# Optimization experiments

Measured on AMD Instinct MI355X. Metric: run time of the kernel, lower is better.

Reference implementation:

```python
import jax, jax.numpy as jnp
import numpy as np

BETA = 0.25

def setup_inputs() -> dict:
    key = jax.random.key(0)
    kz, ke = jax.random.split(key)
    z = jax.random.normal(kz, (8, 256, 8, 32, 32), dtype=jnp.float32)
    num_codes, code_dim = 1024, 256
    # matches nn.init.uniform_(weight, -1/num_codes, 1/num_codes) in scale
    embed = jax.random.uniform(ke, (num_codes, code_dim), dtype=jnp.float32,
                               minval=-1.0 / num_codes, maxval=1.0 / num_codes)
    return {"z": z, "embed": embed}


def reference(z, embed):
    # z: (B, C, D, H, W); embed: (num_codes, code_dim) with C == code_dim
    B, C, D, H, W = z.shape
    num_codes = embed.shape[0]
    z_flat = jnp.transpose(z, (0, 2, 3, 4, 1)).reshape(-1, C)  # (N, C)

    # squared euclidean distances to all codes: ||z||^2 + ||e||^2 - 2 z.e
    dist = ((z_flat * z_flat).sum(axis=1, keepdims=True)
            + (embed * embed).sum(axis=1)
            - 2.0 * z_flat @ embed.T)  # (N, num_codes)
    indices = jnp.argmin(dist, axis=1)  # (N,) int
    z_q_flat = embed[indices]  # (N, C) gather

    # commitment loss (codebook is EMA-updated, so only beta * commitment)
    commitment = jnp.mean((z_flat - jax.lax.stop_gradient(z_q_flat)) ** 2)
    loss = BETA * commitment

    # straight-through estimator
    z_q_flat = z_flat + jax.lax.stop_gradient(z_q_flat - z_flat)
    z_q = jnp.transpose(z_q_flat.reshape(B, D, H, W, C), (0, 4, 1, 2, 3))

    # perplexity (scatter-add histogram instead of materializing one-hot)
    counts = jnp.zeros((num_codes,), dtype=z.dtype).at[indices].add(1.0)
    avg_probs = counts / indices.shape[0]
    perplexity = jnp.exp(-jnp.sum(avg_probs * jnp.log(avg_probs + 1e-10)))

    return z_q, indices.reshape(B, D, H, W), loss, perplexity
```

## Files before the change

### kernel.cpp

```cpp
#include <hip/hip_runtime.h>
#include <math.h>

#define Cdim   256
#define Ssp    8192
#define Npts   65536
#define NCODES 1024
#define BETA   0.25f
#define MT     128
#define NKC    48
#define ESCALE 8192.0f
#define WS_NEED (65536 + (size_t)786432 * 2)

typedef _Float16 f16;
typedef f16   half8  __attribute__((ext_vector_type(8)));
typedef float f32x16 __attribute__((ext_vector_type(16)));

#define MFMA16(A, B, C) __builtin_amdgcn_mfma_f32_32x32x16_f16(A, B, C, 0, 0, 0)

__global__ __launch_bounds__(256) void enorm_kernel(const float* __restrict__ embed,
                                                    float* __restrict__ enorm) {
    int j = blockIdx.x * 256 + threadIdx.x;
    if (j >= NCODES) return;
    const float4* row = reinterpret_cast<const float4*>(embed + (size_t)j * Cdim);
    float s = 0.f;
#pragma unroll 8
    for (int c4 = 0; c4 < Cdim / 4; ++c4) {
        float4 v = row[c4];
        s += v.x * v.x + v.y * v.y + v.z * v.z + v.w * v.w;
    }
    enorm[j] = s;
}

__global__ __launch_bounds__(256) void prep_kernel(const float* __restrict__ embed,
                                                   f16* __restrict__ Bws) {
    int tid = blockIdx.x * 256 + threadIdx.x;
    int o4 = tid * 4;
    int kc = o4 >> 14;
    int r  = o4 & 16383;
    int j  = r >> 4;
    int k0 = r & 15;
#pragma unroll
    for (int i = 0; i < 4; ++i) {
        int k = kc * 16 + k0 + i;
        int c = k & 255;
        float ev = embed[j * 256 + c] * ESCALE;
        f16 eh = (f16)ev;
        f16 v  = (k >= 256 && k < 512) ? (f16)(ev - (float)eh) : eh;
        Bws[o4 + i] = v;
    }
}

#define GG(k) (((k) < 16) ? (2 * (k) + kb) : ((k) < 32) ? (2 * ((k) - 16) + kb) \
                                                        : (32 + 2 * ((k) - 32) + kb))

__global__ __launch_bounds__(512, 2) void vq_gemm(const float* __restrict__ z,
                                                  const f16* __restrict__ Bws,
                                                  const float* __restrict__ enorm,
                                                  float* __restrict__ out_idx,
                                                  float* __restrict__ loss_acc,
                                                  float* __restrict__ counts) {
    __shared__ __attribute__((aligned(16))) f16 As[MT * 512];
    __shared__ float en_s[NCODES];
    __shared__ float znp[4 * MT];
    __shared__ float zn_s[MT];
    __shared__ float redv[8 * MT];
    __shared__ int   redi[8 * MT];

    const int t  = threadIdx.x;
    const int l  = t & 63;
    const int w  = t >> 6;
    const int wm = w >> 2;
    const int wn = w & 3;
    const int ln = l & 31;
    const int kb = l >> 5;
    const int n0 = blockIdx.x * MT;
    const int b  = n0 >> 13;
    const int s0 = n0 & 8191;

    {
        const int p = t & 127;
        const int q = t >> 7;
        const float* zb = z + (size_t)b * ((size_t)Cdim * Ssp) + s0;
        float zsq = 0.f;
#pragma unroll
        for (int gi = 0; gi < 8; ++gi) {
            const int c0 = q * 64 + gi * 8;
            half8 hh, ll;
#pragma unroll
            for (int u = 0; u < 8; ++u) {
                float zv = zb[(size_t)(c0 + u) * Ssp + p];
                zsq += zv * zv;
                f16 zh = (f16)zv;
                hh[u] = zh;
                ll[u] = (f16)(zv - (float)zh);
            }
            const int g0 = c0 >> 3;
            *(half8*)&As[p * 512 + 8 * (g0 ^ (p & 7))]        = hh;
            *(half8*)&As[p * 512 + 8 * ((32 + g0) ^ (p & 7))] = ll;
        }
        znp[q * MT + p] = zsq;
    }
    for (int i = t; i < NCODES; i += 512) en_s[i] = enorm[i];
    __syncthreads();
    if (t < MT)
        zn_s[t] = ((znp[t] + znp[MT + t]) + znp[2 * MT + t]) + znp[3 * MT + t];
    __syncthreads();

#pragma unroll 1
    for (int jh = 0; jh < 2; ++jh) {
        f32x16 acc[2][4] = {};
        const f16* bbase = Bws + (size_t)(jh * 512 + wn * 128 + ln) * 16 + kb * 8;

        half8 b0 = *(const half8*)(bbase);
        half8 b1 = *(const half8*)(bbase + 512);
        half8 b2 = *(const half8*)(bbase + 1024);
        half8 b3 = *(const half8*)(bbase + 1536);

        const int rowA = wm * 64 + ln;
#pragma unroll 2
        for (int kc = 0; kc < NKC; ++kc) {
            const int gg  = GG(kc);
            const int gsw = 8 * (gg ^ (ln & 7));
            half8 a0 = *(const half8*)&As[rowA * 512 + gsw];
            half8 a1 = *(const half8*)&As[(rowA + 32) * 512 + gsw];

            half8 n0r = b0, n1 = b1, n2 = b2, n3 = b3;
            if (kc + 1 < NKC) {
                const f16* src = bbase + (size_t)(kc + 1) * 16384;
                n0r = *(const half8*)(src);
                n1  = *(const half8*)(src + 512);
                n2  = *(const half8*)(src + 1024);
                n3  = *(const half8*)(src + 1536);
            }
            acc[0][0] = MFMA16(a0, b0, acc[0][0]);
            acc[1][0] = MFMA16(a1, b0, acc[1][0]);
            acc[0][1] = MFMA16(a0, b1, acc[0][1]);
            acc[1][1] = MFMA16(a1, b1, acc[1][1]);
            acc[0][2] = MFMA16(a0, b2, acc[0][2]);
            acc[1][2] = MFMA16(a1, b2, acc[1][2]);
            acc[0][3] = MFMA16(a0, b3, acc[0][3]);
            acc[1][3] = MFMA16(a1, b3, acc[1][3]);
            b0 = n0r; b1 = n1; b2 = n2; b3 = n3;
        }

        const int h = l >> 5;
#pragma unroll
        for (int mm = 0; mm < 2; ++mm) {
#pragma unroll
            for (int rg = 0; rg < 16; ++rg) {
                const int row = wm * 64 + mm * 32 + (rg & 3) + 8 * (rg >> 2) + 4 * h;
                const float znv = zn_s[row];
                float bv = 3.0e38f; int bi = 0;
#pragma unroll
                for (int nn = 0; nn < 4; ++nn) {
                    const int col = jh * 512 + wn * 128 + nn * 32 + ln;
                    float k1 = znv + en_s[col];
                    float sc = k1 - acc[mm][nn][rg] * (2.0f / ESCALE);
                    if (sc < bv) { bv = sc; bi = col; }
                }
#pragma unroll
                for (int off = 1; off < 32; off <<= 1) {
                    float ov = __shfl_xor(bv, off, 64);
                    int   oi = __shfl_xor(bi, off, 64);
                    if (ov < bv || (ov == bv && oi < bi)) { bv = ov; bi = oi; }
                }
                if (ln == 0) {
                    redv[(jh * 4 + wn) * MT + row] = bv;
                    redi[(jh * 4 + wn) * MT + row] = bi;
                }
            }
        }
    }
    __syncthreads();

    if (t < MT) {
        float bv = redv[t]; int bi = redi[t];
#pragma unroll
        for (int s = 1; s < 8; ++s) {
            float ov = redv[s * MT + t]; int oi = redi[s * MT + t];
            if (ov < bv || (ov == bv && oi < bi)) { bv = ov; bi = oi; }
        }
        out_idx[n0 + t] = (float)bi;
        atomicAdd(&counts[bi], 1.0f);
        float lsum = bv;
#pragma unroll
        for (int off = 32; off > 0; off >>= 1) lsum += __shfl_down(lsum, off, 64);
        if ((t & 63) == 0) atomicAdd(loss_acc, lsum);
    }
}

__global__ __launch_bounds__(256) void vq_epi(const float* __restrict__ embed,
                                              const float* __restrict__ out_idx,
                                              float* __restrict__ out_zq) {
    const int n = blockIdx.x * 256 + threadIdx.x;
    const int b = n >> 13, s = n & 8191;
    const int idx = (int)out_idx[n];
    const float4* er = reinterpret_cast<const float4*>(embed + (size_t)idx * Cdim);
    float* oq = out_zq + (size_t)b * ((size_t)Cdim * Ssp) + s;
#pragma unroll 4
    for (int c4 = 0; c4 < Cdim / 4; ++c4) {
        float4 e = er[c4];
        const int c = c4 * 4;
        __builtin_nontemporal_store(e.x, oq + (size_t)(c + 0) * Ssp);
        __builtin_nontemporal_store(e.y, oq + (size_t)(c + 1) * Ssp);
        __builtin_nontemporal_store(e.z, oq + (size_t)(c + 2) * Ssp);
        __builtin_nontemporal_store(e.w, oq + (size_t)(c + 3) * Ssp);
    }
}

#define PTS 64
#define CT  128
#define KC  32
__global__ __launch_bounds__(256, 2) void vq_main_fb(const float* __restrict__ z,
                                                     const float* __restrict__ embed,
                                                     const float* __restrict__ enorm,
                                                     float* __restrict__ out_zq,
                                                     float* __restrict__ out_idx,
                                                     float* __restrict__ loss_acc,
                                                     float* __restrict__ counts) {
    __shared__ __attribute__((aligned(16))) float smem[Cdim * PTS + KC * CT];
    float* zt = smem;
    float* et = smem + Cdim * PTS;
    const int t  = threadIdx.x;
    const int n0 = blockIdx.x * PTS;
    const int b  = n0 >> 13;
    const int s0 = n0 & 8191;
    const float* zb = z + (size_t)b * Cdim * Ssp + s0;
    {
        const int p4 = (t & 15) * 4, crow = t >> 4;
#pragma unroll
        for (int it = 0; it < 16; ++it) {
            int c = it * 16 + crow;
            float4 v = *reinterpret_cast<const float4*>(zb + (size_t)c * Ssp + p4);
            *reinterpret_cast<float4*>(&zt[c * PTS + p4]) = v;
        }
    }
    __syncthreads();
    {
        const int p = t & 63, qq = t >> 6;
        float sacc = 0.f;
#pragma unroll 8
        for (int c = qq * 64; c < qq * 64 + 64; ++c) { float v = zt[c * PTS + p]; sacc += v * v; }
        et[qq * 64 + p] = sacc;
    }
    __syncthreads();
    const int pg = t & 15, jg = t >> 4;
    const int p0 = pg * 4;
    float zn[4];
#pragma unroll
    for (int i = 0; i < 4; ++i) {
        int p = p0 + i;
        zn[i] = ((et[p] + et[64 + p]) + et[128 + p]) + et[192 + p];
    }
    float bestv[4] = {3.0e38f, 3.0e38f, 3.0e38f, 3.0e38f};
    int   besti[4] = {0, 0, 0, 0};
    const int dj = t >> 3, q = t & 7;
    const int sw_st = (q & 3) << 3;
    for (int jt = 0; jt < NCODES / CT; ++jt) {
        const int J0 = jt * CT;
        float acc[4][8];
#pragma unroll
        for (int i = 0; i < 4; ++i)
#pragma unroll
            for (int m = 0; m < 8; ++m) acc[i][m] = 0.f;
        for (int ks = 0; ks < Cdim / KC; ++ks) {
            const int cc0 = ks * KC;
            __syncthreads();
#pragma unroll
            for (int i = 0; i < 4; ++i) {
                const int jrel = dj + 32 * i;
                const float4 v = *reinterpret_cast<const float4*>(
                    embed + (size_t)(J0 + jrel) * Cdim + cc0 + q * 4);
                const int c0 = q * 4;
                const int jsw = jrel ^ sw_st;
                et[(c0 + 0) * CT + jsw] = v.x;
                et[(c0 + 1) * CT + jsw] = v.y;
                et[(c0 + 2) * CT + jsw] = v.z;
                et[(c0 + 3) * CT + jsw] = v.w;
            }
            __syncthreads();
#pragma unroll 4
            for (int c = 0; c < KC; ++c) {
                const float4 zp = *reinterpret_cast<const float4*>(&zt[(cc0 + c) * PTS + p0]);
                const int jb = (jg * 8) ^ (((c >> 2) & 3) << 3);
                const float4 ea = *reinterpret_cast<const float4*>(&et[c * CT + jb]);
                const float4 eb = *reinterpret_cast<const float4*>(&et[c * CT + jb + 4]);
                const float zc[4] = {zp.x, zp.y, zp.z, zp.w};
                const float ec[8] = {ea.x, ea.y, ea.z, ea.w, eb.x, eb.y, eb.z, eb.w};
#pragma unroll
                for (int i = 0; i < 4; ++i)
#pragma unroll
                    for (int m = 0; m < 8; ++m) acc[i][m] += zc[i] * ec[m];
            }
        }
#pragma unroll
        for (int m = 0; m < 8; ++m) {
            const int cid = J0 + jg * 8 + m;
            const float en = enorm[cid];
#pragma unroll
            for (int i = 0; i < 4; ++i) {
                float k1 = zn[i] + en;
                float sc = k1 - 2.0f * acc[i][m];
                if (sc < bestv[i]) { bestv[i] = sc; besti[i] = cid; }
            }
        }
    }
    __syncthreads();
    float* rv = et; int* ri = (int*)(et + 1024); int* idxf = (int*)(et + 2048);
#pragma unroll
    for (int i = 0; i < 4; ++i) { int p = p0 + i; rv[p * 16 + jg] = bestv[i]; ri[p * 16 + jg] = besti[i]; }
    __syncthreads();
    if (t < PTS) {
        int p = t;
        float bv = rv[p * 16]; int bi = ri[p * 16];
        for (int g = 1; g < 16; ++g) {
            float v = rv[p * 16 + g]; int ii = ri[p * 16 + g];
            if (v < bv || (v == bv && ii < bi)) { bv = v; bi = ii; }
        }
        idxf[p] = bi;
        out_idx[n0 + p] = (float)bi;
        atomicAdd(&counts[bi], 1.0f);
    }
    __syncthreads();
    float lsum = 0.f;
    {
        const int p = t & 63, cbase = t >> 6;
        const int myidx = idxf[p];
        const float4* erow4 = reinterpret_cast<const float4*>(embed + (size_t)myidx * Cdim);
        float* ob = out_zq + (size_t)b * Cdim * Ssp + s0 + p;
#pragma unroll 4
        for (int pass = 0; pass < 16; ++pass) {
            int c = cbase * 64 + pass * 4;
            float4 e = erow4[c >> 2];
            ob[(size_t)(c + 0) * Ssp] = e.x;
            ob[(size_t)(c + 1) * Ssp] = e.y;
            ob[(size_t)(c + 2) * Ssp] = e.z;
            ob[(size_t)(c + 3) * Ssp] = e.w;
            float d0 = zt[(c + 0) * PTS + p] - e.x;
            float d1 = zt[(c + 1) * PTS + p] - e.y;
            float d2 = zt[(c + 2) * PTS + p] - e.z;
            float d3 = zt[(c + 3) * PTS + p] - e.w;
            lsum += d0 * d0 + d1 * d1 + d2 * d2 + d3 * d3;
        }
    }
#pragma unroll
    for (int off = 32; off > 0; off >>= 1) lsum += __shfl_down(lsum, off, 64);
    if ((t & 63) == 0) atomicAdd(loss_acc, lsum);
}

__global__ __launch_bounds__(1024) void vq_final(const float* __restrict__ counts,
                                                 const float* __restrict__ loss_acc,
                                                 float* __restrict__ out_loss,
                                                 float* __restrict__ out_perp) {
    __shared__ float red[16];
    int t = threadIdx.x;
    float cnt = counts[t];
    float avg = cnt * (1.0f / (float)Npts);
    float term = avg * logf(avg + 1e-10f);
#pragma unroll
    for (int off = 32; off > 0; off >>= 1) term += __shfl_down(term, off, 64);
    if ((t & 63) == 0) red[t >> 6] = term;
    __syncthreads();
    if (t == 0) {
        float s = 0.f;
        for (int i = 0; i < 16; ++i) s += red[i];
        *out_perp = expf(-s);
        *out_loss = BETA * loss_acc[0] * (1.0f / 16777216.0f);
    }
}

extern "C" void kernel_launch(void* const* d_in, const int* in_sizes, int n_in,
                              void* d_out, int out_size, void* d_ws, size_t ws_size,
                              hipStream_t stream) {
    const float* z     = (const float*)d_in[0];
    const float* embed = (const float*)d_in[1];

    float* ws       = (float*)d_ws;
    float* loss_acc = ws;
    float* counts   = ws + 64;
    float* enorm    = ws + 2048;

    float* out_zq   = (float*)d_out;
    float* out_idx  = out_zq + (size_t)Npts * Cdim;
    float* out_loss = out_idx + Npts;
    float* out_perp = out_loss + 1;

    hipMemsetAsync(d_ws, 0, 2048 * sizeof(float), stream);
    enorm_kernel<<<NCODES / 256, 256, 0, stream>>>(embed, enorm);

    if (ws_size >= WS_NEED) {
        f16* Bws = (f16*)((char*)d_ws + 65536);
        prep_kernel<<<768, 256, 0, stream>>>(embed, Bws);
        vq_gemm<<<Npts / MT, 512, 0, stream>>>(z, Bws, enorm, out_idx,
                                               loss_acc, counts);
        vq_epi<<<Npts / 256, 256, 0, stream>>>(embed, out_idx, out_zq);
    } else {
        vq_main_fb<<<Npts / PTS, 256, 0, stream>>>(z, embed, enorm, out_zq, out_idx,
                                                   loss_acc, counts);
    }
    vq_final<<<1, 1024, 0, stream>>>(counts, loss_acc, out_loss, out_perp);
}
```

Before: 207.8 us.

## Stage codebook tiles in LDS via async global_load_lds with double buffering

The row tile shrinks from 128 to 64 points per block. Each of the 8 waves now owns 128 codes across all 1024, so the two-pass jh loop goes away. Codebook k-chunks are copied asynchronously into double-buffered, swizzled LDS with global_load_lds and read from there, replacing per-wave direct global loads. This lets the block share B loads and overlap them with MFMA, at the cost of a barrier every k-step and more LDS, which may cut occupancy. z loads also become nontemporal.

```diff
diff --git a/kernel.cpp b/kernel.cpp
--- a/kernel.cpp
+++ b/kernel.cpp
@@ -6,7 +6,7 @@
 #define Npts   65536
 #define NCODES 1024
 #define BETA   0.25f
-#define MT     128
+#define MT     64
 #define NKC    48
 #define ESCALE 8192.0f
 #define WS_NEED (65536 + (size_t)786432 * 2)
@@ -60,8 +60,9 @@
                                                   float* __restrict__ loss_acc,
                                                   float* __restrict__ counts) {
     __shared__ __attribute__((aligned(16))) f16 As[MT * 512];
+    __shared__ __attribute__((aligned(16))) f16 Bt[2][NCODES * 16];
     __shared__ float en_s[NCODES];
-    __shared__ float znp[4 * MT];
+    __shared__ float znp[256];
     __shared__ float zn_s[MT];
     __shared__ float redv[8 * MT];
     __shared__ int   redi[8 * MT];
@@ -69,17 +70,41 @@
     const int t  = threadIdx.x;
     const int l  = t & 63;
     const int w  = t >> 6;
-    const int wm = w >> 2;
-    const int wn = w & 3;
     const int ln = l & 31;
     const int kb = l >> 5;
     const int n0 = blockIdx.x * MT;
     const int b  = n0 >> 13;
     const int s0 = n0 & 8191;
 
-    {
-        const int p = t & 127;
-        const int q = t >> 7;
+    int srcel[4];
+#pragma unroll
+    for (int i = 0; i < 4; ++i) {
+        const int s   = i * 512 + t;
+        const int o   = s * 16;
+        const int jq  = o >> 7;
+        const int lin = o ^ ((jq & 3) << 4);
+        const int j   = lin >> 5;
+        const int kb2 = (lin >> 4) & 1;
+        srcel[i] = j * 16 + kb2 * 8;
+    }
+
+#define STAGEB(kcn, bufi)                                                          \
+    {                                                                              \
+        const f16* srcb = Bws + (size_t)(kcn) * 16384;                             \
+        _Pragma("unroll")                                                          \
+        for (int i = 0; i < 4; ++i) {                                              \
+            __builtin_amdgcn_global_load_lds(                                      \
+                (const __attribute__((address_space(1))) unsigned int*)(srcb + srcel[i]), \
+                (__attribute__((address_space(3))) unsigned int*)&Bt[(bufi)][(size_t)(i * 512 + t) * 8], \
+                16, 0, 0);                                                         \
+        }                                                                          \
+    }
+
+    STAGEB(0, 0)
+
+    if (t < 256) {
+        const int p = t & 63;
+        const int q = t >> 6;
         const float* zb = z + (size_t)b * ((size_t)Cdim * Ssp) + s0;
         float zsq = 0.f;
 #pragma unroll
@@ -88,7 +113,7 @@
             half8 hh, ll;
 #pragma unroll
             for (int u = 0; u < 8; ++u) {
-                float zv = zb[(size_t)(c0 + u) * Ssp + p];
+                float zv = __builtin_nontemporal_load(zb + (size_t)(c0 + u) * Ssp + p);
                 zsq += zv * zv;
                 f16 zh = (f16)zv;
                 hh[u] = zh;
@@ -98,62 +123,48 @@
             *(half8*)&As[p * 512 + 8 * (g0 ^ (p & 7))]        = hh;
             *(half8*)&As[p * 512 + 8 * ((32 + g0) ^ (p & 7))] = ll;
         }
-        znp[q * MT + p] = zsq;
+        znp[q * 64 + p] = zsq;
     }
     for (int i = t; i < NCODES; i += 512) en_s[i] = enorm[i];
     __syncthreads();
-    if (t < MT)
-        zn_s[t] = ((znp[t] + znp[MT + t]) + znp[2 * MT + t]) + znp[3 * MT + t];
-    __syncthreads();
-
+    if (t < MT) zn_s[t] = ((znp[t] + znp[64 + t]) + znp[128 + t]) + znp[192 + t];
+
+    const int jlane  = w * 128 + ln;
+    const int bbyte0 = (jlane * 32 + kb * 16) ^ (((jlane >> 2) & 3) << 4);
+    __syncthreads();
+
+    f32x16 acc[2][4] = {};
 #pragma unroll 1
-    for (int jh = 0; jh < 2; ++jh) {
-        f32x16 acc[2][4] = {};
-        const f16* bbase = Bws + (size_t)(jh * 512 + wn * 128 + ln) * 16 + kb * 8;
-
-        half8 b0 = *(const half8*)(bbase);
-        half8 b1 = *(const half8*)(bbase + 512);
-        half8 b2 = *(const half8*)(bbase + 1024);
-        half8 b3 = *(const half8*)(bbase + 1536);
-
-        const int rowA = wm * 64 + ln;
-#pragma unroll 2
-        for (int kc = 0; kc < NKC; ++kc) {
-            const int gg  = GG(kc);
-            const int gsw = 8 * (gg ^ (ln & 7));
-            half8 a0 = *(const half8*)&As[rowA * 512 + gsw];
-            half8 a1 = *(const half8*)&As[(rowA + 32) * 512 + gsw];
-
-            half8 n0r = b0, n1 = b1, n2 = b2, n3 = b3;
-            if (kc + 1 < NKC) {
-                const f16* src = bbase + (size_t)(kc + 1) * 16384;
-                n0r = *(const half8*)(src);
-                n1  = *(const half8*)(src + 512);
-                n2  = *(const half8*)(src + 1024);
-                n3  = *(const half8*)(src + 1536);
-            }
-            acc[0][0] = MFMA16(a0, b0, acc[0][0]);
-            acc[1][0] = MFMA16(a1, b0, acc[1][0]);
-            acc[0][1] = MFMA16(a0, b1, acc[0][1]);
-            acc[1][1] = MFMA16(a1, b1, acc[1][1]);
-            acc[0][2] = MFMA16(a0, b2, acc[0][2]);
-            acc[1][2] = MFMA16(a1, b2, acc[1][2]);
-            acc[0][3] = MFMA16(a0, b3, acc[0][3]);
-            acc[1][3] = MFMA16(a1, b3, acc[1][3]);
-            b0 = n0r; b1 = n1; b2 = n2; b3 = n3;
-        }
-
+    for (int kc = 0; kc < NKC; ++kc) {
+        const int cur = kc & 1;
+        if (kc + 1 < NKC) STAGEB(kc + 1, cur ^ 1)
+
+        const int gg  = GG(kc);
+        const int gsw = 8 * (gg ^ (ln & 7));
+        half8 a0 = *(const half8*)&As[ln * 512 + gsw];
+        half8 a1 = *(const half8*)&As[(32 + ln) * 512 + gsw];
+        const char* bbuf = (const char*)&Bt[cur][0];
+#pragma unroll
+        for (int nn = 0; nn < 4; ++nn) {
+            half8 bf = *(const half8*)(bbuf + bbyte0 + nn * 1024);
+            acc[0][nn] = MFMA16(a0, bf, acc[0][nn]);
+            acc[1][nn] = MFMA16(a1, bf, acc[1][nn]);
+        }
+        __syncthreads();
+    }
+
+    {
         const int h = l >> 5;
 #pragma unroll
         for (int mm = 0; mm < 2; ++mm) {
 #pragma unroll
             for (int rg = 0; rg < 16; ++rg) {
-                const int row = wm * 64 + mm * 32 + (rg & 3) + 8 * (rg >> 2) + 4 * h;
+                const int row = mm * 32 + (rg & 3) + 8 * (rg >> 2) + 4 * h;
                 const float znv = zn_s[row];
                 float bv = 3.0e38f; int bi = 0;
 #pragma unroll
                 for (int nn = 0; nn < 4; ++nn) {
-                    const int col = jh * 512 + wn * 128 + nn * 32 + ln;
+                    const int col = w * 128 + nn * 32 + ln;
                     float k1 = znv + en_s[col];
                     float sc = k1 - acc[mm][nn][rg] * (2.0f / ESCALE);
                     if (sc < bv) { bv = sc; bi = col; }
@@ -165,8 +176,8 @@
                     if (ov < bv || (ov == bv && oi < bi)) { bv = ov; bi = oi; }
                 }
                 if (ln == 0) {
-                    redv[(jh * 4 + wn) * MT + row] = bv;
-                    redi[(jh * 4 + wn) * MT + row] = bi;
+                    redv[w * MT + row] = bv;
+                    redi[w * MT + row] = bi;
                 }
             }
         }
@@ -187,6 +198,7 @@
         for (int off = 32; off > 0; off >>= 1) lsum += __shfl_down(lsum, off, 64);
         if ((t & 63) == 0) atomicAdd(loss_acc, lsum);
     }
+#undef STAGEB
 }
 
 __global__ __launch_bounds__(256) void vq_epi(const float* __restrict__ embed,
```

Result: slower. 246.3 us (+18.5%).
